# Optimization experiments

Hardware: AMD Instinct MI355X
Metric: run time of the kernel (lower is better)

The kernel has to match this reference:

```python
import jax, jax.numpy as jnp
import numpy as np

HIDDEN = 10

def setup_inputs() -> dict:
    key = jax.random.key(0)
    ks = jax.random.split(key, 8)
    B, T = 4096, 512
    scale = 1.0 / np.sqrt(HIDDEN)  # torch LSTM/Linear default init range
    x = jax.random.normal(ks[0], (B, T, 1), dtype=jnp.float32)
    h0 = jnp.zeros((1, B, HIDDEN), dtype=jnp.float32)
    c0 = jnp.zeros((1, B, HIDDEN), dtype=jnp.float32)
    # LSTM params, gate order i, f, g, o (torch convention)
    W_ih = jax.random.uniform(ks[1], (4 * HIDDEN, 1), minval=-scale, maxval=scale, dtype=jnp.float32)
    W_hh = jax.random.uniform(ks[2], (4 * HIDDEN, HIDDEN), minval=-scale, maxval=scale, dtype=jnp.float32)
    b_ih = jax.random.uniform(ks[3], (4 * HIDDEN,), minval=-scale, maxval=scale, dtype=jnp.float32)
    b_hh = jax.random.uniform(ks[4], (4 * HIDDEN,), minval=-scale, maxval=scale, dtype=jnp.float32)
    W1 = jax.random.uniform(ks[5], (HIDDEN, HIDDEN), minval=-scale, maxval=scale, dtype=jnp.float32)
    b1 = jax.random.uniform(ks[6], (HIDDEN,), minval=-scale, maxval=scale, dtype=jnp.float32)
    W2 = jax.random.uniform(ks[7], (1, HIDDEN), minval=-scale, maxval=scale, dtype=jnp.float32)
    b2 = jnp.zeros((1,), dtype=jnp.float32)
    return {"x": x, "h0": h0, "c0": c0, "W_ih": W_ih, "W_hh": W_hh,
            "b_ih": b_ih, "b_hh": b_hh, "W1": W1, "b1": b1, "W2": W2, "b2": b2}

def _lstm_scan(x_tbi, h, c, W_ih, W_hh, b):
    # x_tbi: [T, B, 1]; h, c: [B, H]; W_ih: [4H, 1]; W_hh: [4H, H]; b: [4H]
    def step(carry, xt):
        h, c = carry
        gates = xt @ W_ih.T + h @ W_hh.T + b  # [B, 4H]
        i, f, g, o = jnp.split(gates, 4, axis=-1)
        c_new = jax.nn.sigmoid(f) * c + jax.nn.sigmoid(i) * jnp.tanh(g)
        h_new = jax.nn.sigmoid(o) * jnp.tanh(c_new)
        return (h_new, c_new), h_new
    (_, _), hs = jax.lax.scan(step, (h, c), x_tbi)
    return hs  # [T, B, H]

def reference(x, h0, c0, W_ih, W_hh, b_ih, b_hh, W1, b1, W2, b2):
    # x: [B, T, 1] (batch_first); h0, c0: [1, B, H]
    x_tbi = jnp.transpose(x, (1, 0, 2))  # [T, B, 1]
    hs = _lstm_scan(x_tbi, h0[0], c0[0], W_ih, W_hh, b_ih + b_hh)  # [T, B, H]
    out = jnp.transpose(hs, (1, 0, 2))  # [B, T, H]
    reg = jnp.maximum(out @ W1.T + b1, 0.0) @ W2.T + b2  # [B, T, 1]
    return jnp.squeeze(reg + x, axis=2)  # [B, T]
```

## Files before the change

### kernel.cpp

```cpp
#include <hip/hip_runtime.h>

#define BB 4096
#define TT 512
#define HH 10
#define L2E 1.44269504088896340736f

typedef __fp16 half2_t __attribute__((ext_vector_type(2)));

__device__ __forceinline__ float rcp_(float x) { return __builtin_amdgcn_rcpf(x); }
__device__ __forceinline__ float exp2_(float x) { return __builtin_amdgcn_exp2f(x); }

template <int CTRL, int BANK = 0xF>
__device__ __forceinline__ int dppi_(int old, int src) {
    return __builtin_amdgcn_update_dpp(old, src, CTRL, 0xF, BANK, true);
}
template <int CTRL>
__device__ __forceinline__ float dpp_(float v) {
    return __int_as_float(__builtin_amdgcn_update_dpp(
        0, __float_as_int(v), CTRL, 0xF, 0xF, true));
}
#define QP_XOR1 0xB1
#define QP_XOR2 0x4E
#define QP_B0   0x00
#define QP_B2   0xAA
#define ROR4    0x124
#define ROR8    0x128
#define ROR12   0x12C

__global__ __launch_bounds__(64) void lstm16dpp2_kernel(
    const float* __restrict__ x, const float* __restrict__ h0, const float* __restrict__ c0,
    const float* __restrict__ W_ih, const float* __restrict__ W_hh,
    const float* __restrict__ b_ih, const float* __restrict__ b_hh,
    const float* __restrict__ W1, const float* __restrict__ b1,
    const float* __restrict__ W2, const float* __restrict__ b2,
    float* __restrict__ out)
{
    const int lane = threadIdx.x;
    const int l = lane & 15;
    const int e = blockIdx.x * 4 + (lane >> 4);

    const bool owner = (l < HH);
    const int u = owner ? l : 0;
    const float m = owner ? 1.0f : 0.0f;

    const int ri = u, rf = 10 + u, rg = 20 + u, ro = 30 + u;
    const float sS = -L2E;
    const float sG = -2.0f * L2E;
    half2_t Wi[5], Wf[5], Wg[5], Wo[5];
    {
        const float2* pi = (const float2*)(W_hh + ri * HH);
        const float2* pf = (const float2*)(W_hh + rf * HH);
        const float2* pg = (const float2*)(W_hh + rg * HH);
        const float2* po = (const float2*)(W_hh + ro * HH);
#pragma unroll
        for (int p = 0; p < 5; p++) {
            float2 wi = pi[p], wf = pf[p], wg = pg[p], wo = po[p];
            Wi[p] = __builtin_amdgcn_cvt_pkrtz(wi.x * m * sS, wi.y * m * sS);
            Wf[p] = __builtin_amdgcn_cvt_pkrtz(wf.x * m * sS, wf.y * m * sS);
            Wg[p] = __builtin_amdgcn_cvt_pkrtz(wg.x * m * sG, wg.y * m * sG);
            Wo[p] = __builtin_amdgcn_cvt_pkrtz(wo.x * m * sS, wo.y * m * sS);
        }
    }
    const float bi = (b_ih[ri] + b_hh[ri]) * sS;
    const float bf = (b_ih[rf] + b_hh[rf]) * sS;
    const float bg = (b_ih[rg] + b_hh[rg]) * sG;
    const float bo = (b_ih[ro] + b_hh[ro]) * sS;
    const float wii = W_ih[ri] * sS, wif = W_ih[rf] * sS;
    const float wig = W_ih[rg] * sG, wio = W_ih[ro] * sS;

    half2_t W1p[5];
    {
        const float2* rp = (const float2*)(W1 + u * HH);
#pragma unroll
        for (int p = 0; p < 5; p++) {
            float2 w = rp[p];
            W1p[p] = __builtin_amdgcn_cvt_pkrtz(w.x * m, w.y * m);
        }
    }
    const float b1r = m * b1[u];
    const float W2r = m * W2[u];
    const float seedb = (l == 0) ? b2[0] : 0.0f;

    const bool oddlane = (lane & 1);

    float c = owner ? c0[e * HH + u] : 0.0f;
    half2_t hp[5];
    {
        float hb[10];
#pragma unroll
        for (int j = 0; j < 10; j++) hb[j] = h0[e * HH + j];
#pragma unroll
        for (int p = 0; p < 5; p++) hp[p] = __builtin_amdgcn_cvt_pkrtz(hb[2 * p], hb[2 * p + 1]);
    }

    const float4* xq  = (const float4*)(x + (size_t)e * TT);
    float4*       ob4 = (float4*)(out + (size_t)e * TT);

    float4 xc = xq[0];
    for (int gb = 0; gb < TT / 4; gb++) {
        const int gbn = (gb + 1) & (TT / 4 - 1);
        float4 xn = xq[gbn];
        float4 outv;

#pragma unroll
        for (int r4 = 0; r4 < 4; r4++) {
            const float xv = (r4 == 0) ? xc.x : (r4 == 1) ? xc.y : (r4 == 2) ? xc.z : xc.w;

            float gi = fmaf(xv, wii, bi);
            float gf = fmaf(xv, wif, bf);
            float gg = fmaf(xv, wig, bg);
            float go = fmaf(xv, wio, bo);
#pragma unroll
            for (int p = 0; p < 5; p++) {
                gi = __builtin_amdgcn_fdot2(hp[p], Wi[p], gi, false);
                gf = __builtin_amdgcn_fdot2(hp[p], Wf[p], gf, false);
                gg = __builtin_amdgcn_fdot2(hp[p], Wg[p], gg, false);
                go = __builtin_amdgcn_fdot2(hp[p], Wo[p], go, false);
            }
            const float A = exp2_(gi);
            const float F = exp2_(gf);
            const float G = exp2_(gg);
            const float O = exp2_(go);

            const float af = rcp_(1.0f + F);
            const float q  = (1.0f - G) * rcp_((1.0f + A) * (1.0f + G));
            const float cn = fmaf(af, c, q);
            c = cn;
            const float T  = exp2_(cn * (-2.0f * L2E));
            const float hq = (1.0f - T) * rcp_((1.0f + O) * (1.0f + T));

            const float hq_p = dpp_<QP_XOR1>(hq);
            const float plo = oddlane ? hq_p : hq;
            const float phi = oddlane ? hq : hq_p;
            half2_t pkh = __builtin_amdgcn_cvt_pkrtz(plo, phi);
            const int pk = *(const int*)&pkh;
            const int A_ = dppi_<QP_B0>(0, pk);
            const int B_ = dppi_<QP_B2>(0, pk);
            int h0i = A_;
            h0i = dppi_<ROR12, 0x2>(h0i, A_);
            h0i = dppi_<ROR8,  0x4>(h0i, A_);
            h0i = dppi_<ROR4,  0x8>(h0i, A_);
            int h1i = B_;
            h1i = dppi_<ROR12, 0x2>(h1i, B_);
            h1i = dppi_<ROR8,  0x4>(h1i, B_);
            h1i = dppi_<ROR4,  0x8>(h1i, B_);
            int h2i = A_;
            h2i = dppi_<ROR4,  0x1>(h2i, A_);
            h2i = dppi_<ROR12, 0x4>(h2i, A_);
            h2i = dppi_<ROR8,  0x8>(h2i, A_);
            int h3i = B_;
            h3i = dppi_<ROR4,  0x1>(h3i, B_);
            h3i = dppi_<ROR12, 0x4>(h3i, B_);
            h3i = dppi_<ROR8,  0x8>(h3i, B_);
            int h4i = A_;
            h4i = dppi_<ROR8,  0x1>(h4i, A_);
            h4i = dppi_<ROR4,  0x2>(h4i, A_);
            h4i = dppi_<ROR12, 0x8>(h4i, A_);
            hp[0] = *(const half2_t*)&h0i;
            hp[1] = *(const half2_t*)&h1i;
            hp[2] = *(const half2_t*)&h2i;
            hp[3] = *(const half2_t*)&h3i;
            hp[4] = *(const half2_t*)&h4i;

            float a = b1r;
#pragma unroll
            for (int p = 0; p < 5; p++)
                a = __builtin_amdgcn_fdot2(hp[p], W1p[p], a, false);
            float part = fmaf(fmaxf(a, 0.0f), W2r, seedb);
            part += dpp_<QP_XOR1>(part);
            part += dpp_<QP_XOR2>(part);
            part += dpp_<ROR4>(part);
            part += dpp_<ROR8>(part);
            const float s = part + xv;

            if (r4 == 0) outv.x = s;
            else if (r4 == 1) outv.y = s;
            else if (r4 == 2) outv.z = s;
            else outv.w = s;
        }

        if (l == 0) ob4[gb] = outv;
        xc = xn;
    }
}

extern "C" void kernel_launch(void* const* d_in, const int* in_sizes, int n_in,
                              void* d_out, int out_size, void* d_ws, size_t ws_size,
                              hipStream_t stream) {
    const float* x    = (const float*)d_in[0];
    const float* h0   = (const float*)d_in[1];
    const float* c0   = (const float*)d_in[2];
    const float* W_ih = (const float*)d_in[3];
    const float* W_hh = (const float*)d_in[4];
    const float* b_ih = (const float*)d_in[5];
    const float* b_hh = (const float*)d_in[6];
    const float* W1   = (const float*)d_in[7];
    const float* b1   = (const float*)d_in[8];
    const float* W2   = (const float*)d_in[9];
    const float* b2   = (const float*)d_in[10];
    float* out = (float*)d_out;

    dim3 grid(BB * 16 / 64);
    dim3 block(64);
    lstm16dpp2_kernel<<<grid, block, 0, stream>>>(x, h0, c0, W_ih, W_hh, b_ih, b_hh,
                                                  W1, b1, W2, b2, out);
}
```

Measured before the change: 117.3 us.

## Software-pipeline regressor head one step behind recurrence and trim DPP broadcasts

The ReLU/Linear head for step t-1 now runs right after the gate dot products of step t, so it can interleave with the serial LSTM transcendental chain instead of trailing it. Outputs are stored one float4 group late, and an epilogue computes and writes the final timestep. The h-broadcast also drops the odd-lane select and the last DPP per packed vector, because lanes 12-15 only multiply zero-masked weights. This shortens the per-step dependency chain, at the cost of an extra epilogue and delayed stores.

```diff
diff --git a/kernel.cpp b/kernel.cpp
--- a/kernel.cpp
+++ b/kernel.cpp
@@ -27,7 +27,7 @@
 #define ROR8    0x128
 #define ROR12   0x12C
 
-__global__ __launch_bounds__(64) void lstm16dpp2_kernel(
+__global__ __launch_bounds__(64) void lstm16pipe_kernel(
     const float* __restrict__ x, const float* __restrict__ h0, const float* __restrict__ c0,
     const float* __restrict__ W_ih, const float* __restrict__ W_hh,
     const float* __restrict__ b_ih, const float* __restrict__ b_hh,
@@ -81,8 +81,6 @@
     const float W2r = m * W2[u];
     const float seedb = (l == 0) ? b2[0] : 0.0f;
 
-    const bool oddlane = (lane & 1);
-
     float c = owner ? c0[e * HH + u] : 0.0f;
     half2_t hp[5];
     {
@@ -97,10 +95,12 @@
     float4*       ob4 = (float4*)(out + (size_t)e * TT);
 
     float4 xc = xq[0];
+    float4 outv;
+    float xprev = 0.0f;
+
     for (int gb = 0; gb < TT / 4; gb++) {
         const int gbn = (gb + 1) & (TT / 4 - 1);
         float4 xn = xq[gbn];
-        float4 outv;
 
 #pragma unroll
         for (int r4 = 0; r4 < 4; r4++) {
@@ -117,11 +117,31 @@
                 gg = __builtin_amdgcn_fdot2(hp[p], Wg[p], gg, false);
                 go = __builtin_amdgcn_fdot2(hp[p], Wo[p], go, false);
             }
+
+            {
+                float a = b1r;
+#pragma unroll
+                for (int p = 0; p < 5; p++)
+                    a = __builtin_amdgcn_fdot2(hp[p], W1p[p], a, false);
+                float part = fmaf(fmaxf(a, 0.0f), W2r, seedb);
+                part += dpp_<QP_XOR1>(part);
+                part += dpp_<QP_XOR2>(part);
+                part += dpp_<ROR4>(part);
+                part += dpp_<ROR8>(part);
+                const float s = part + xprev;
+                if (r4 == 0) {
+                    outv.w = s;
+                    if (gb && l == 0) ob4[gb - 1] = outv;
+                }
+                else if (r4 == 1) outv.x = s;
+                else if (r4 == 2) outv.y = s;
+                else outv.z = s;
+            }
+
             const float A = exp2_(gi);
             const float F = exp2_(gf);
             const float G = exp2_(gg);
             const float O = exp2_(go);
-
             const float af = rcp_(1.0f + F);
             const float q  = (1.0f - G) * rcp_((1.0f + A) * (1.0f + G));
             const float cn = fmaf(af, c, q);
@@ -130,57 +150,49 @@
             const float hq = (1.0f - T) * rcp_((1.0f + O) * (1.0f + T));
 
             const float hq_p = dpp_<QP_XOR1>(hq);
-            const float plo = oddlane ? hq_p : hq;
-            const float phi = oddlane ? hq : hq_p;
-            half2_t pkh = __builtin_amdgcn_cvt_pkrtz(plo, phi);
+            half2_t pkh = __builtin_amdgcn_cvt_pkrtz(hq, hq_p);
             const int pk = *(const int*)&pkh;
             const int A_ = dppi_<QP_B0>(0, pk);
             const int B_ = dppi_<QP_B2>(0, pk);
             int h0i = A_;
             h0i = dppi_<ROR12, 0x2>(h0i, A_);
             h0i = dppi_<ROR8,  0x4>(h0i, A_);
-            h0i = dppi_<ROR4,  0x8>(h0i, A_);
             int h1i = B_;
             h1i = dppi_<ROR12, 0x2>(h1i, B_);
             h1i = dppi_<ROR8,  0x4>(h1i, B_);
-            h1i = dppi_<ROR4,  0x8>(h1i, B_);
             int h2i = A_;
             h2i = dppi_<ROR4,  0x1>(h2i, A_);
             h2i = dppi_<ROR12, 0x4>(h2i, A_);
-            h2i = dppi_<ROR8,  0x8>(h2i, A_);
             int h3i = B_;
             h3i = dppi_<ROR4,  0x1>(h3i, B_);
             h3i = dppi_<ROR12, 0x4>(h3i, B_);
-            h3i = dppi_<ROR8,  0x8>(h3i, B_);
             int h4i = A_;
             h4i = dppi_<ROR8,  0x1>(h4i, A_);
             h4i = dppi_<ROR4,  0x2>(h4i, A_);
-            h4i = dppi_<ROR12, 0x8>(h4i, A_);
             hp[0] = *(const half2_t*)&h0i;
             hp[1] = *(const half2_t*)&h1i;
             hp[2] = *(const half2_t*)&h2i;
             hp[3] = *(const half2_t*)&h3i;
             hp[4] = *(const half2_t*)&h4i;
 
-            float a = b1r;
-#pragma unroll
-            for (int p = 0; p < 5; p++)
-                a = __builtin_amdgcn_fdot2(hp[p], W1p[p], a, false);
-            float part = fmaf(fmaxf(a, 0.0f), W2r, seedb);
-            part += dpp_<QP_XOR1>(part);
-            part += dpp_<QP_XOR2>(part);
-            part += dpp_<ROR4>(part);
-            part += dpp_<ROR8>(part);
-            const float s = part + xv;
-
-            if (r4 == 0) outv.x = s;
-            else if (r4 == 1) outv.y = s;
-            else if (r4 == 2) outv.z = s;
-            else outv.w = s;
+            xprev = xv;
         }
 
-        if (l == 0) ob4[gb] = outv;
         xc = xn;
+    }
+
+    {
+        float a = b1r;
+#pragma unroll
+        for (int p = 0; p < 5; p++)
+            a = __builtin_amdgcn_fdot2(hp[p], W1p[p], a, false);
+        float part = fmaf(fmaxf(a, 0.0f), W2r, seedb);
+        part += dpp_<QP_XOR1>(part);
+        part += dpp_<QP_XOR2>(part);
+        part += dpp_<ROR4>(part);
+        part += dpp_<ROR8>(part);
+        outv.w = part + xprev;
+        if (l == 0) ob4[TT / 4 - 1] = outv;
     }
 }
 
@@ -202,6 +214,6 @@
 
     dim3 grid(BB * 16 / 64);
     dim3 block(64);
-    lstm16dpp2_kernel<<<grid, block, 0, stream>>>(x, h0, c0, W_ih, W_hh, b_ih, b_hh,
+    lstm16pipe_kernel<<<grid, block, 0, stream>>>(x, h0, c0, W_ih, W_hh, b_ih, b_hh,
                                                   W1, b1, W2, b2, out);
 }
```

Measured after the change: 97.43 us (median of 2 runs). 17.0% less time.
